# Performance work log

Hardware: AMD Instinct MI355X
Metric: run time of the kernel (lower is better)

## Reference

```python
import jax, jax.numpy as jnp
import numpy as np

L, B, N, C, H = 6, 4, 512, 512, 8
D = C // H          # head_dim = 64
MLP = 4 * C         # mlp_ratio = 4.0
EPS = 1e-6


def setup_inputs() -> dict:
    key = jax.random.key(0)
    ks = jax.random.split(key, 12)
    p = lambda k, sh: jax.random.normal(k, sh, dtype=jnp.float32) * 0.02
    return {
        "x": jax.random.normal(ks[0], (B, N, C), dtype=jnp.float32),
        "time_emb": jax.random.normal(ks[1], (B, C), dtype=jnp.float32),
        "pair_emb": jax.random.normal(ks[2], (B, H, N, N), dtype=jnp.float32) * 0.1,
        "is_padded_mask": jnp.zeros((B, 1, 1, N), dtype=bool),
        # per-block stacked params (leading dim = L blocks)
        "wq": p(ks[3], (L, C, C)),
        "wk": p(ks[4], (L, C, C)),
        "wv": p(ks[5], (L, C, C)),
        "wo": p(ks[6], (L, C, C)),
        "bo": jnp.zeros((L, C), dtype=jnp.float32),
        "w1": p(ks[7], (L, C, MLP)),
        "b1": jnp.zeros((L, MLP), dtype=jnp.float32),
        "w2": p(ks[8], (L, MLP, C)),
        "b2": jnp.zeros((L, C), dtype=jnp.float32),
        "wada": p(ks[9], (L, C, 6 * C)),
        "bada": jnp.zeros((L, 6 * C), dtype=jnp.float32),
    }


def _ln(x):
    # LayerNorm without affine, eps=1e-6 (torch elementwise_affine=False)
    mu = jnp.mean(x, axis=-1, keepdims=True)
    var = jnp.mean(jnp.square(x - mu), axis=-1, keepdims=True)
    return (x - mu) * jax.lax.rsqrt(var + EPS)


def _modulate(x, shift, scale):
    return x * (1.0 + scale[:, None, :]) + shift[:, None, :]


def reference(x, time_emb, pair_emb, is_padded_mask,
              wq, wk, wv, wo, bo, w1, b1, w2, b2, wada, bada):
    scale = D ** -0.5
    t_act = jax.nn.silu(time_emb)  # shared SiLU input to adaLN of each block
    for i in range(L):
        ada = t_act @ wada[i] + bada[i]  # (B, 6C)
        sh_msa, sc_msa, g_msa, sh_mlp, sc_mlp, g_mlp = jnp.split(ada, 6, axis=1)
        # fill_attn_mask: masked_fill padded key positions with -inf
        pair = jnp.where(is_padded_mask, -jnp.inf, pair_emb)  # (B,H,N,N)
        mx = _modulate(_ln(x), sh_msa, sc_msa)  # (B,N,C)
        q = (mx @ wq[i]).reshape(B, N, H, D)
        k = (mx @ wk[i]).reshape(B, N, H, D)
        v = (mx @ wv[i]).reshape(B, N, H, D)
        qk = jnp.einsum('bnhd,bshd->bhns', q, k) * scale  # (B,H,N,N)
        attn = jax.nn.softmax(qk + pair, axis=-1)
        o = jnp.einsum('bhns,bshd->bnhd', attn, v).reshape(B, N, C)
        o = o @ wo[i] + bo[i]
        x = x + g_msa[:, None, :] * o
        pair_emb = pair + qk  # residual on pair embedding
        h = _modulate(_ln(x), sh_mlp, sc_mlp)
        h = jax.nn.gelu(h @ w1[i] + b1[i], approximate=True) @ w2[i] + b2[i]
        x = x + g_mlp[:, None, :] * h
    return x, pair_emb
```

## Files before the change

### kernel.cpp

```cpp
#include <hip/hip_runtime.h>
#include <hip/hip_bf16.h>

#define LNUM 6
#define BB 4
#define NSEQ 512
#define CDIM 512
#define HNUM 8
#define DHEAD 64
#define MLPD 2048
#define MROWS (BB*NSEQ)

typedef __hip_bfloat16 bf16;
typedef __attribute__((ext_vector_type(4))) float f32x4;
typedef __attribute__((ext_vector_type(8))) short bf16x8;

__device__ __forceinline__ void gld_lds16(const bf16* g, bf16* l) {
  __builtin_amdgcn_global_load_lds((const __attribute__((address_space(1))) void*)g,
                                   (__attribute__((address_space(3))) void*)l, 16, 0, 0);
}

__device__ __forceinline__ short f2bs(float f) {
  bf16 h = __float2bfloat16(f);
  short s; __builtin_memcpy(&s, &h, 2); return s;
}

__device__ __forceinline__ float gelu_tanh(float t) {
  float u = 0.7978845608028654f * (t + 0.044715f * t * t * t);
  u = fminf(fmaxf(u, -15.f), 15.f);
  float e = __expf(2.f * u);
  return 0.5f * t * (1.f + (e - 1.f) / (e + 1.f));
}

enum { EP_BF16 = 0, EP_SCORES = 1, EP_RESID = 2, EP_GELU = 3 };

template<int MODE>
__global__ __launch_bounds__(256) void gemm_nt(
    const bf16* __restrict__ A, int lda,
    const bf16* __restrict__ Bt, int ldb,
    int K, int zdiv,
    long sA1, long sA2, long sB1, long sB2, long sO1, long sO2,
    bf16* __restrict__ obf, float* __restrict__ of32, int ldo,
    const float* __restrict__ bias,
    const float* __restrict__ ada, int gate_off,
    float* __restrict__ xres,
    const float* __restrict__ pair_in,
    const unsigned char* __restrict__ mask,
    float scale)
{
  __shared__ bf16 lA[2 * 64 * 64];
  __shared__ bf16 lB[2 * 64 * 64];
  const int tid = threadIdx.x;
  const int wid = tid >> 6, lane = tid & 63;
  const int z = blockIdx.z;
  const long z1 = z / zdiv, z2 = z % zdiv;
  A  += z1 * sA1 + z2 * sA2;
  Bt += z1 * sB1 + z2 * sB2;
  const long obase = z1 * sO1 + z2 * sO2;
  const int m0 = blockIdx.x * 64;
  const int n0 = blockIdx.y * 64;
  const int wm = wid >> 1, wn = wid & 1;
  const int srow = tid >> 3, scl = tid & 7;

  f32x4 zero = {0.f, 0.f, 0.f, 0.f};
  f32x4 acc[2][2];
#pragma unroll
  for (int i = 0; i < 2; i++)
#pragma unroll
    for (int j = 0; j < 2; j++) acc[i][j] = zero;

  auto stage = [&](int buf, int kt) {
#pragma unroll
    for (int r = 0; r < 2; r++) {
      const int rr = (r << 5) + srow;
      const int gk = (scl ^ (rr & 7)) << 3;
      gld_lds16(A + (size_t)(m0 + rr) * lda + (kt << 6) + gk,
                lA + buf * 4096 + (r << 11) + (wid << 9));
    }
#pragma unroll
    for (int r = 0; r < 2; r++) {
      const int rr = (r << 5) + srow;
      const int gk = (scl ^ (rr & 7)) << 3;
      gld_lds16(Bt + (size_t)(n0 + rr) * ldb + (kt << 6) + gk,
                lB + buf * 4096 + (r << 11) + (wid << 9));
    }
  };

  const int rlo = lane & 15, kq = lane >> 4;
  auto compute = [&](int buf) {
    bf16x8 af[2][2], bg[2][2];
#pragma unroll
    for (int kk = 0; kk < 2; kk++) {
#pragma unroll
      for (int i = 0; i < 2; i++) {
        const int ra = (wm << 5) + (i << 4) + rlo;
        af[kk][i] = *(const bf16x8*)(lA + buf * 4096 + (ra << 6) +
                                     ((((kk << 2) + kq) ^ (ra & 7)) << 3));
        const int rb2 = (wn << 5) + (i << 4) + rlo;
        bg[kk][i] = *(const bf16x8*)(lB + buf * 4096 + (rb2 << 6) +
                                     ((((kk << 2) + kq) ^ (rb2 & 7)) << 3));
      }
    }
#pragma unroll
    for (int kk = 0; kk < 2; kk++)
#pragma unroll
      for (int i = 0; i < 2; i++)
#pragma unroll
        for (int j = 0; j < 2; j++)
          acc[i][j] = __builtin_amdgcn_mfma_f32_16x16x32_bf16(af[kk][i], bg[kk][j], acc[i][j], 0, 0, 0);
  };

  const int NT = K >> 6;
  stage(0, 0);
  for (int t = 0; t < NT - 1; t++) {
    stage((t + 1) & 1, t + 1);
    asm volatile("s_waitcnt vmcnt(4)" ::: "memory");
    __builtin_amdgcn_s_barrier();
    asm volatile("" ::: "memory");
    compute(t & 1);
    asm volatile("" ::: "memory");
    __builtin_amdgcn_s_barrier();
  }
  asm volatile("s_waitcnt vmcnt(0)" ::: "memory");
  __builtin_amdgcn_s_barrier();
  asm volatile("" ::: "memory");
  compute((NT - 1) & 1);

  const int cl = lane & 15, rb = (lane >> 4) << 2;
#pragma unroll
  for (int i = 0; i < 2; i++) {
#pragma unroll
    for (int j = 0; j < 2; j++) {
      const int gc = n0 + (wn << 5) + (j << 4) + cl;
#pragma unroll
      for (int r = 0; r < 4; r++) {
        const int gr = m0 + (wm << 5) + (i << 4) + rb + r;
        float v = acc[i][j][r];
        if (MODE == EP_BF16) {
          obf[obase + (size_t)gr * ldo + gc] = __float2bfloat16(v);
        } else if (MODE == EP_SCORES) {
          float pr = pair_in[obase + (size_t)gr * ldo + gc];
          if (mask[z1 * NSEQ + gc]) pr = -INFINITY;
          of32[obase + (size_t)gr * ldo + gc] = pr + v * scale;
        } else if (MODE == EP_RESID) {
          const int b = gr >> 9;
          float t2 = v + bias[gc];
          xres[(size_t)gr * CDIM + gc] += ada[b * (6 * CDIM) + gate_off + gc] * t2;
        } else {
          float t2 = v + bias[gc];
          obf[obase + (size_t)gr * ldo + gc] = __float2bfloat16(gelu_tanh(t2));
        }
      }
    }
  }
}

__global__ __launch_bounds__(256) void ln_mod(const float* __restrict__ x,
                                              const float* __restrict__ ada,
                                              int sh_off, int sc_off,
                                              bf16* __restrict__ out)
{
  const int row = blockIdx.x;
  const int b = row >> 9;
  const float* xr = x + (size_t)row * CDIM;
  const int t = threadIdx.x;
  float2 v = ((const float2*)xr)[t];
  float s = v.x + v.y;
  float ss = v.x * v.x + v.y * v.y;
#pragma unroll
  for (int o = 32; o > 0; o >>= 1) { s += __shfl_down(s, o); ss += __shfl_down(ss, o); }
  __shared__ float red[8];
  __shared__ float mv[2];
  const int w = t >> 6, ln = t & 63;
  if (ln == 0) { red[w] = s; red[4 + w] = ss; }
  __syncthreads();
  if (t == 0) {
    float S = red[0] + red[1] + red[2] + red[3];
    float SS = red[4] + red[5] + red[6] + red[7];
    float mu = S * (1.0f / CDIM);
    float var = SS * (1.0f / CDIM) - mu * mu;
    mv[0] = mu; mv[1] = rsqrtf(var + 1e-6f);
  }
  __syncthreads();
  const float mu = mv[0], rs = mv[1];
  const float* adab = ada + b * (6 * CDIM);
  const int c = t * 2;
  float o0 = (v.x - mu) * rs * (1.0f + adab[sc_off + c])     + adab[sh_off + c];
  float o1 = (v.y - mu) * rs * (1.0f + adab[sc_off + c + 1]) + adab[sh_off + c + 1];
  out[(size_t)row * CDIM + c]     = __float2bfloat16(o0);
  out[(size_t)row * CDIM + c + 1] = __float2bfloat16(o1);
}

__global__ __launch_bounds__(256) void ada_gemm(const float* __restrict__ te,
                                                const float* __restrict__ wada,
                                                const float* __restrict__ bada,
                                                float* __restrict__ out)
{
  __shared__ float ta[CDIM];
  const int layer = blockIdx.y;
  const float* wada_i = wada + (size_t)layer * CDIM * 6 * CDIM;
  const float* bada_i = bada + (size_t)layer * 6 * CDIM;
  float* out_i = out + (size_t)layer * BB * 6 * CDIM;
  const int idx = blockIdx.x * 256 + threadIdx.x;
  const int b = idx / (6 * CDIM);
  const int col = idx % (6 * CDIM);
  for (int i = threadIdx.x; i < CDIM; i += 256) {
    float xx = te[b * CDIM + i];
    ta[i] = xx / (1.f + __expf(-xx));
  }
  __syncthreads();
  float acc = bada_i[col];
#pragma unroll 8
  for (int k = 0; k < CDIM; k++)
    acc = fmaf(ta[k], wada_i[(size_t)k * (6 * CDIM) + col], acc);
  out_i[idx] = acc;
}

__global__ __launch_bounds__(64) void softmax_rows(const float* __restrict__ S,
                                                   bf16* __restrict__ P)
{
  const size_t row = blockIdx.x;
  const float* sr = S + row * NSEQ;
  const int t = threadIdx.x;
  float4 a = ((const float4*)sr)[t];
  float4 b = ((const float4*)sr)[t + 64];
  float m = fmaxf(fmaxf(fmaxf(a.x, a.y), fmaxf(a.z, a.w)),
                  fmaxf(fmaxf(b.x, b.y), fmaxf(b.z, b.w)));
#pragma unroll
  for (int o = 32; o > 0; o >>= 1) m = fmaxf(m, __shfl_xor(m, o));
  float e0 = __expf(a.x - m), e1 = __expf(a.y - m), e2 = __expf(a.z - m), e3 = __expf(a.w - m);
  float e4 = __expf(b.x - m), e5 = __expf(b.y - m), e6 = __expf(b.z - m), e7 = __expf(b.w - m);
  float sum = (e0 + e1 + e2 + e3) + (e4 + e5 + e6 + e7);
#pragma unroll
  for (int o = 32; o > 0; o >>= 1) sum += __shfl_xor(sum, o);
  const float inv = 1.0f / sum;
  short4 w0, w1;
  w0.x = f2bs(e0 * inv); w0.y = f2bs(e1 * inv); w0.z = f2bs(e2 * inv); w0.w = f2bs(e3 * inv);
  w1.x = f2bs(e4 * inv); w1.y = f2bs(e5 * inv); w1.z = f2bs(e6 * inv); w1.w = f2bs(e7 * inv);
  bf16* pr = P + row * NSEQ;
  ((short4*)pr)[t] = w0;
  ((short4*)pr)[t + 64] = w1;
}

__global__ __launch_bounds__(256) void conv_t(const float* __restrict__ src, bf16* __restrict__ dst,
                                              int R, int Ccols, long sS, long sD)
{
  src += (size_t)blockIdx.z * sS;
  dst += (size_t)blockIdx.z * sD;
  __shared__ float tb[32][33];
  const int c0 = blockIdx.x * 32, r0 = blockIdx.y * 32;
  const int tx = threadIdx.x & 31, ty = threadIdx.x >> 5;
#pragma unroll
  for (int i = ty; i < 32; i += 8) tb[i][tx] = src[(size_t)(r0 + i) * Ccols + c0 + tx];
  __syncthreads();
#pragma unroll
  for (int i = ty; i < 32; i += 8) dst[(size_t)(c0 + i) * R + r0 + tx] = __float2bfloat16(tb[tx][i]);
}

__global__ __launch_bounds__(256) void vtrans(const bf16* __restrict__ qkv, bf16* __restrict__ vt)
{
  const int z = blockIdx.z, b = z >> 3, h = z & 7;
  const bf16* src = qkv + (size_t)b * NSEQ * 1536 + 2 * CDIM + h * DHEAD;
  bf16* dst = vt + (size_t)z * DHEAD * NSEQ;
  __shared__ bf16 tb[32][33];
  const int n0 = blockIdx.x * 32, d0 = blockIdx.y * 32;
  const int tx = threadIdx.x & 31, ty = threadIdx.x >> 5;
#pragma unroll
  for (int i = ty; i < 32; i += 8) tb[i][tx] = src[(size_t)(n0 + i) * 1536 + d0 + tx];
  __syncthreads();
#pragma unroll
  for (int i = ty; i < 32; i += 8) dst[(size_t)(d0 + i) * NSEQ + n0 + tx] = tb[tx][i];
}

extern "C" void kernel_launch(void* const* d_in, const int* in_sizes, int n_in,
                              void* d_out, int out_size, void* d_ws, size_t ws_size,
                              hipStream_t stream)
{
  (void)in_sizes; (void)n_in; (void)out_size; (void)ws_size;
  const float* in_x    = (const float*)d_in[0];
  const float* in_te   = (const float*)d_in[1];
  const float* in_pair = (const float*)d_in[2];
  const unsigned char* in_mask = (const unsigned char*)d_in[3];
  const float* wq   = (const float*)d_in[4];
  const float* wk   = (const float*)d_in[5];
  const float* wv   = (const float*)d_in[6];
  const float* wo   = (const float*)d_in[7];
  const float* bo   = (const float*)d_in[8];
  const float* w1   = (const float*)d_in[9];
  const float* b1   = (const float*)d_in[10];
  const float* w2   = (const float*)d_in[11];
  const float* b2   = (const float*)d_in[12];
  const float* wada = (const float*)d_in[13];
  const float* bada = (const float*)d_in[14];

  float* xout = (float*)d_out;
  float* pairout = xout + (size_t)BB * NSEQ * CDIM;

  char* ws = (char*)d_ws;
  size_t off = 0;
  auto alloc = [&](size_t bytes) -> void* {
    void* p = ws + off; off += (bytes + 255) & ~(size_t)255; return p;
  };
  bf16*  wqkvT = (bf16*)alloc((size_t)LNUM * 1536 * 512 * 2);
  bf16*  woT   = (bf16*)alloc((size_t)LNUM * 512 * 512 * 2);
  bf16*  w1T   = (bf16*)alloc((size_t)LNUM * 2048 * 512 * 2);
  bf16*  w2T   = (bf16*)alloc((size_t)LNUM * 512 * 2048 * 2);
  float* adab  = (float*)alloc((size_t)LNUM * BB * 6 * CDIM * 4);
  bf16*  mx    = (bf16*)alloc((size_t)MROWS * CDIM * 2);
  bf16*  qkv   = (bf16*)alloc((size_t)MROWS * 1536 * 2);
  bf16*  vt    = (bf16*)alloc((size_t)BB * HNUM * DHEAD * NSEQ * 2);
  bf16*  Pbuf  = (bf16*)alloc((size_t)BB * HNUM * NSEQ * NSEQ * 2);
  bf16*  obuf  = (bf16*)alloc((size_t)MROWS * CDIM * 2);
  bf16*  hbuf  = (bf16*)alloc((size_t)MROWS * MLPD * 2);

  hipMemcpyAsync(xout, in_x, (size_t)MROWS * CDIM * 4, hipMemcpyDeviceToDevice, stream);

  conv_t<<<dim3(16, 16, LNUM), 256, 0, stream>>>(wq, wqkvT,               512, 512,  (long)512 * 512,  (long)1536 * 512);
  conv_t<<<dim3(16, 16, LNUM), 256, 0, stream>>>(wk, wqkvT + 512 * 512,   512, 512,  (long)512 * 512,  (long)1536 * 512);
  conv_t<<<dim3(16, 16, LNUM), 256, 0, stream>>>(wv, wqkvT + 2 * 512 * 512, 512, 512, (long)512 * 512, (long)1536 * 512);
  conv_t<<<dim3(16, 16, LNUM), 256, 0, stream>>>(wo, woT,                 512, 512,  (long)512 * 512,  (long)512 * 512);
  conv_t<<<dim3(64, 16, LNUM), 256, 0, stream>>>(w1, w1T,                 512, 2048, (long)512 * 2048, (long)2048 * 512);
  conv_t<<<dim3(16, 64, LNUM), 256, 0, stream>>>(w2, w2T,                 2048, 512, (long)2048 * 512, (long)512 * 2048);

  ada_gemm<<<dim3(BB * 6 * CDIM / 256, LNUM), 256, 0, stream>>>(in_te, wada, bada, adab);

  const float scale = 0.125f;
  for (int i = 0; i < LNUM; i++) {
    const float* adal = adab + (size_t)i * BB * 6 * CDIM;
    ln_mod<<<MROWS, 256, 0, stream>>>(xout, adal, 0, CDIM, mx);
    gemm_nt<EP_BF16><<<dim3(32, 24, 1), 256, 0, stream>>>(
        mx, CDIM, wqkvT + (size_t)i * 1536 * 512, CDIM, CDIM, 1,
        0, 0, 0, 0, 0, 0,
        qkv, nullptr, 1536,
        nullptr, nullptr, 0, nullptr, nullptr, nullptr, 0.f);
    vtrans<<<dim3(16, 2, 32), 256, 0, stream>>>(qkv, vt);
    const float* pin = (i == 0) ? in_pair : pairout;
    gemm_nt<EP_SCORES><<<dim3(8, 8, 32), 256, 0, stream>>>(
        qkv, 1536, qkv + CDIM, 1536, DHEAD, HNUM,
        (long)NSEQ * 1536, 64, (long)NSEQ * 1536, 64,
        (long)HNUM * NSEQ * NSEQ, (long)NSEQ * NSEQ,
        nullptr, pairout, NSEQ,
        nullptr, nullptr, 0, nullptr, pin, in_mask, scale);
    softmax_rows<<<dim3(BB * HNUM * NSEQ), 64, 0, stream>>>(pairout, Pbuf);
    gemm_nt<EP_BF16><<<dim3(8, 1, 32), 256, 0, stream>>>(
        Pbuf, NSEQ, vt, NSEQ, NSEQ, HNUM,
        (long)HNUM * NSEQ * NSEQ, (long)NSEQ * NSEQ,
        (long)HNUM * DHEAD * NSEQ, (long)DHEAD * NSEQ,
        (long)NSEQ * CDIM, DHEAD,
        obuf, nullptr, CDIM,
        nullptr, nullptr, 0, nullptr, nullptr, nullptr, 0.f);
    gemm_nt<EP_RESID><<<dim3(32, 8, 1), 256, 0, stream>>>(
        obuf, CDIM, woT + (size_t)i * CDIM * CDIM, CDIM, CDIM, 1,
        0, 0, 0, 0, 0, 0,
        nullptr, nullptr, CDIM,
        bo + (size_t)i * CDIM, adal, 2 * CDIM, xout, nullptr, nullptr, 0.f);
    ln_mod<<<MROWS, 256, 0, stream>>>(xout, adal, 3 * CDIM, 4 * CDIM, mx);
    gemm_nt<EP_GELU><<<dim3(32, 32, 1), 256, 0, stream>>>(
        mx, CDIM, w1T + (size_t)i * MLPD * CDIM, CDIM, CDIM, 1,
        0, 0, 0, 0, 0, 0,
        hbuf, nullptr, MLPD,
        b1 + (size_t)i * MLPD, nullptr, 0, nullptr, nullptr, nullptr, 0.f);
    gemm_nt<EP_RESID><<<dim3(32, 8, 1), 256, 0, stream>>>(
        hbuf, MLPD, w2T + (size_t)i * CDIM * MLPD, MLPD, MLPD, 1,
        0, 0, 0, 0, 0, 0,
        nullptr, nullptr, CDIM,
        b2 + (size_t)i * CDIM, adal, 5 * CDIM, xout, nullptr, nullptr, 0.f);
  }
}
```

Baseline: 615.3 us.

## Fuse attention scores, online softmax and PV into one flash-style kernel

Replaces the separate scores GEMM, row softmax and P·V GEMM with one kernel per (batch, head, 64-row tile). The kernel streams K/V tiles through double-buffered LDS, adds the pair bias, writes the updated pair embedding, and accumulates the output with an online softmax. This removes the bf16 P round-trip through global memory and two launches per layer. The adaLN GEMM is also split over K into partial and reduce kernels to get more parallelism. The fused grid has only 256 blocks, so the GPU may be undersubscribed.

```diff
diff --git a/kernel.cpp b/kernel.cpp
--- a/kernel.cpp
+++ b/kernel.cpp
@@ -31,7 +31,7 @@
   return 0.5f * t * (1.f + (e - 1.f) / (e + 1.f));
 }
 
-enum { EP_BF16 = 0, EP_SCORES = 1, EP_RESID = 2, EP_GELU = 3 };
+enum { EP_BF16 = 0, EP_RESID = 2, EP_GELU = 3 };
 
 template<int MODE>
 __global__ __launch_bounds__(256) void gemm_nt(
@@ -39,13 +39,10 @@
     const bf16* __restrict__ Bt, int ldb,
     int K, int zdiv,
     long sA1, long sA2, long sB1, long sB2, long sO1, long sO2,
-    bf16* __restrict__ obf, float* __restrict__ of32, int ldo,
+    bf16* __restrict__ obf, int ldo,
     const float* __restrict__ bias,
     const float* __restrict__ ada, int gate_off,
-    float* __restrict__ xres,
-    const float* __restrict__ pair_in,
-    const unsigned char* __restrict__ mask,
-    float scale)
+    float* __restrict__ xres)
 {
   __shared__ bf16 lA[2 * 64 * 64];
   __shared__ bf16 lB[2 * 64 * 64];
@@ -137,10 +134,6 @@
         float v = acc[i][j][r];
         if (MODE == EP_BF16) {
           obf[obase + (size_t)gr * ldo + gc] = __float2bfloat16(v);
-        } else if (MODE == EP_SCORES) {
-          float pr = pair_in[obase + (size_t)gr * ldo + gc];
-          if (mask[z1 * NSEQ + gc]) pr = -INFINITY;
-          of32[obase + (size_t)gr * ldo + gc] = pr + v * scale;
         } else if (MODE == EP_RESID) {
           const int b = gr >> 9;
           float t2 = v + bias[gc];
@@ -152,6 +145,160 @@
       }
     }
   }
+}
+
+__global__ __launch_bounds__(256) void attn_fused(
+    const bf16* __restrict__ qkv, const bf16* __restrict__ vt,
+    const float* __restrict__ pair_in, float* __restrict__ pair_out,
+    const unsigned char* __restrict__ mask,
+    bf16* __restrict__ obuf, float scale)
+{
+  __shared__ bf16 lQ[64 * 64];
+  __shared__ bf16 lK[2][64 * 64];
+  __shared__ bf16 lV[2][64 * 64];
+  __shared__ bf16 lP[64 * 64];
+  const int tid = threadIdx.x, wid = tid >> 6, lane = tid & 63;
+  const int z = blockIdx.z, b = z >> 3, h = z & 7;
+  const int m0 = blockIdx.x * 64;
+  const int srow = tid >> 3, scl = tid & 7;
+  const bf16* Aq = qkv + (size_t)b * NSEQ * 1536 + h * 64;
+  const bf16* Bk = Aq + CDIM;
+  const bf16* Bv = vt + (size_t)z * DHEAD * NSEQ;
+  const size_t pz = (size_t)z * NSEQ * NSEQ;
+
+#pragma unroll
+  for (int r = 0; r < 2; r++) {
+    const int rr = (r << 5) + srow;
+    const int gk = (scl ^ (rr & 7)) << 3;
+    gld_lds16(Aq + (size_t)(m0 + rr) * 1536 + gk, lQ + (r << 11) + (wid << 9));
+    gld_lds16(Bk + (size_t)rr * 1536 + gk, lK[0] + (r << 11) + (wid << 9));
+    gld_lds16(Bv + (size_t)rr * NSEQ + gk, lV[0] + (r << 11) + (wid << 9));
+  }
+
+  const int rlo = lane & 15, kq = lane >> 4, cl = rlo;
+  float m_run[4], l_run[4];
+  f32x4 oacc[4];
+  f32x4 zero = {0.f, 0.f, 0.f, 0.f};
+#pragma unroll
+  for (int r = 0; r < 4; r++) { m_run[r] = -INFINITY; l_run[r] = 0.f; }
+#pragma unroll
+  for (int j = 0; j < 4; j++) oacc[j] = zero;
+  bf16x8 afq[2];
+
+  for (int ct = 0; ct < 8; ct++) {
+    const int cur = ct & 1;
+    asm volatile("s_waitcnt vmcnt(0)" ::: "memory");
+    __builtin_amdgcn_s_barrier();
+    asm volatile("" ::: "memory");
+
+    if (ct < 7) {
+#pragma unroll
+      for (int r = 0; r < 2; r++) {
+        const int rr = (r << 5) + srow;
+        const int gk = (scl ^ (rr & 7)) << 3;
+        gld_lds16(Bk + (size_t)((ct + 1) * 64 + rr) * 1536 + gk,
+                  lK[cur ^ 1] + (r << 11) + (wid << 9));
+        gld_lds16(Bv + (size_t)rr * NSEQ + (ct + 1) * 64 + gk,
+                  lV[cur ^ 1] + (r << 11) + (wid << 9));
+      }
+    }
+
+    if (ct == 0) {
+#pragma unroll
+      for (int kk = 0; kk < 2; kk++) {
+        const int ra = (wid << 4) + rlo;
+        afq[kk] = *(const bf16x8*)(lQ + (ra << 6) + ((((kk << 1) << 1) + kq) == 0 ? 0 : 0));
+      }
+#pragma unroll
+      for (int kk = 0; kk < 2; kk++) {
+        const int ra = (wid << 4) + rlo;
+        afq[kk] = *(const bf16x8*)(lQ + (ra << 6) + ((((kk << 2) + kq) ^ (ra & 7)) << 3));
+      }
+    }
+
+    float pr[4][4];
+#pragma unroll
+    for (int j = 0; j < 4; j++)
+#pragma unroll
+      for (int r = 0; r < 4; r++)
+        pr[j][r] = pair_in[pz + (size_t)(m0 + (wid << 4) + (kq << 2) + r) * NSEQ +
+                           (ct * 64 + (j << 4) + cl)];
+    bool mk[4];
+#pragma unroll
+    for (int j = 0; j < 4; j++)
+      mk[j] = mask[b * NSEQ + ct * 64 + (j << 4) + cl] != 0;
+
+    f32x4 s[4];
+#pragma unroll
+    for (int j = 0; j < 4; j++) s[j] = zero;
+#pragma unroll
+    for (int kk = 0; kk < 2; kk++)
+#pragma unroll
+      for (int j = 0; j < 4; j++) {
+        const int rk = (j << 4) + rlo;
+        bf16x8 bk = *(const bf16x8*)(lK[cur] + (rk << 6) + ((((kk << 2) + kq) ^ (rk & 7)) << 3));
+        s[j] = __builtin_amdgcn_mfma_f32_16x16x32_bf16(afq[kk], bk, s[j], 0, 0, 0);
+      }
+
+    float p[4][4];
+#pragma unroll
+    for (int r = 0; r < 4; r++) {
+      const size_t prow = pz + (size_t)(m0 + (wid << 4) + (kq << 2) + r) * NSEQ + ct * 64;
+      float sf[4];
+#pragma unroll
+      for (int j = 0; j < 4; j++) {
+        float pp = mk[j] ? -INFINITY : pr[j][r];
+        sf[j] = s[j][r] * scale + pp;
+        pair_out[prow + (j << 4) + cl] = sf[j];
+      }
+      float tm = fmaxf(fmaxf(sf[0], sf[1]), fmaxf(sf[2], sf[3]));
+#pragma unroll
+      for (int o = 1; o < 16; o <<= 1) tm = fmaxf(tm, __shfl_xor(tm, o));
+      const float mnew = fmaxf(m_run[r], tm);
+      const float fr = __expf(m_run[r] - mnew);
+      float rs = 0.f;
+#pragma unroll
+      for (int j = 0; j < 4; j++) { p[j][r] = __expf(sf[j] - mnew); rs += p[j][r]; }
+#pragma unroll
+      for (int o = 1; o < 16; o <<= 1) rs += __shfl_xor(rs, o);
+      l_run[r] = l_run[r] * fr + rs;
+      m_run[r] = mnew;
+#pragma unroll
+      for (int j = 0; j < 4; j++) oacc[j][r] *= fr;
+    }
+
+#pragma unroll
+    for (int j = 0; j < 4; j++)
+#pragma unroll
+      for (int r = 0; r < 4; r++) {
+        const int row = (wid << 4) + (kq << 2) + r;
+        const int col = (j << 4) + cl;
+        lP[(row << 6) + (((col >> 3) ^ (row & 7)) << 3) + (col & 7)] = __float2bfloat16(p[j][r]);
+      }
+    asm volatile("s_waitcnt lgkmcnt(0)" ::: "memory");
+    __builtin_amdgcn_sched_barrier(0);
+
+#pragma unroll
+    for (int kk = 0; kk < 2; kk++) {
+      const int ra = (wid << 4) + rlo;
+      bf16x8 ap = *(const bf16x8*)(lP + (ra << 6) + ((((kk << 2) + kq) ^ (ra & 7)) << 3));
+#pragma unroll
+      for (int j = 0; j < 4; j++) {
+        const int rd = (j << 4) + rlo;
+        bf16x8 bv = *(const bf16x8*)(lV[cur] + (rd << 6) + ((((kk << 2) + kq) ^ (rd & 7)) << 3));
+        oacc[j] = __builtin_amdgcn_mfma_f32_16x16x32_bf16(ap, bv, oacc[j], 0, 0, 0);
+      }
+    }
+  }
+
+#pragma unroll
+  for (int j = 0; j < 4; j++)
+#pragma unroll
+    for (int r = 0; r < 4; r++) {
+      const int gr = m0 + (wid << 4) + (kq << 2) + r;
+      const int gc = h * 64 + (j << 4) + cl;
+      obuf[((size_t)b * NSEQ + gr) * CDIM + gc] = __float2bfloat16(oacc[j][r] / l_run[r]);
+    }
 }
 
 __global__ __launch_bounds__(256) void ln_mod(const float* __restrict__ x,
@@ -190,55 +337,49 @@
   out[(size_t)row * CDIM + c + 1] = __float2bfloat16(o1);
 }
 
-__global__ __launch_bounds__(256) void ada_gemm(const float* __restrict__ te,
+__global__ __launch_bounds__(256) void ada_part(const float* __restrict__ te,
                                                 const float* __restrict__ wada,
-                                                const float* __restrict__ bada,
-                                                float* __restrict__ out)
-{
-  __shared__ float ta[CDIM];
-  const int layer = blockIdx.y;
-  const float* wada_i = wada + (size_t)layer * CDIM * 6 * CDIM;
-  const float* bada_i = bada + (size_t)layer * 6 * CDIM;
-  float* out_i = out + (size_t)layer * BB * 6 * CDIM;
+                                                float* __restrict__ partial)
+{
+  __shared__ float ta[4][64];
+  const int layer = blockIdx.z, kc = blockIdx.y;
+  const int t = threadIdx.x;
+  {
+    const int b = t >> 6, kk = t & 63;
+    float xx = te[b * CDIM + kc * 64 + kk];
+    ta[b][kk] = xx / (1.f + __expf(-xx));
+  }
+  __syncthreads();
+  const int col = blockIdx.x * 512 + t * 2;
+  const float* W = wada + ((size_t)layer * CDIM + kc * 64) * 3072 + col;
+  float2 acc0 = {0, 0}, acc1 = {0, 0}, acc2 = {0, 0}, acc3 = {0, 0};
+#pragma unroll 8
+  for (int kk = 0; kk < 64; kk++) {
+    float2 w = *(const float2*)(W + (size_t)kk * 3072);
+    acc0.x = fmaf(ta[0][kk], w.x, acc0.x); acc0.y = fmaf(ta[0][kk], w.y, acc0.y);
+    acc1.x = fmaf(ta[1][kk], w.x, acc1.x); acc1.y = fmaf(ta[1][kk], w.y, acc1.y);
+    acc2.x = fmaf(ta[2][kk], w.x, acc2.x); acc2.y = fmaf(ta[2][kk], w.y, acc2.y);
+    acc3.x = fmaf(ta[3][kk], w.x, acc3.x); acc3.y = fmaf(ta[3][kk], w.y, acc3.y);
+  }
+  float* pp = partial + (((size_t)(layer * 8 + kc) * 4) * 3072);
+  *(float2*)(pp + 0 * 3072 + col) = acc0;
+  *(float2*)(pp + 1 * 3072 + col) = acc1;
+  *(float2*)(pp + 2 * 3072 + col) = acc2;
+  *(float2*)(pp + 3 * 3072 + col) = acc3;
+}
+
+__global__ __launch_bounds__(256) void ada_reduce(const float* __restrict__ partial,
+                                                  const float* __restrict__ bada,
+                                                  float* __restrict__ adab)
+{
   const int idx = blockIdx.x * 256 + threadIdx.x;
-  const int b = idx / (6 * CDIM);
-  const int col = idx % (6 * CDIM);
-  for (int i = threadIdx.x; i < CDIM; i += 256) {
-    float xx = te[b * CDIM + i];
-    ta[i] = xx / (1.f + __expf(-xx));
-  }
-  __syncthreads();
-  float acc = bada_i[col];
-#pragma unroll 8
-  for (int k = 0; k < CDIM; k++)
-    acc = fmaf(ta[k], wada_i[(size_t)k * (6 * CDIM) + col], acc);
-  out_i[idx] = acc;
-}
-
-__global__ __launch_bounds__(64) void softmax_rows(const float* __restrict__ S,
-                                                   bf16* __restrict__ P)
-{
-  const size_t row = blockIdx.x;
-  const float* sr = S + row * NSEQ;
-  const int t = threadIdx.x;
-  float4 a = ((const float4*)sr)[t];
-  float4 b = ((const float4*)sr)[t + 64];
-  float m = fmaxf(fmaxf(fmaxf(a.x, a.y), fmaxf(a.z, a.w)),
-                  fmaxf(fmaxf(b.x, b.y), fmaxf(b.z, b.w)));
-#pragma unroll
-  for (int o = 32; o > 0; o >>= 1) m = fmaxf(m, __shfl_xor(m, o));
-  float e0 = __expf(a.x - m), e1 = __expf(a.y - m), e2 = __expf(a.z - m), e3 = __expf(a.w - m);
-  float e4 = __expf(b.x - m), e5 = __expf(b.y - m), e6 = __expf(b.z - m), e7 = __expf(b.w - m);
-  float sum = (e0 + e1 + e2 + e3) + (e4 + e5 + e6 + e7);
-#pragma unroll
-  for (int o = 32; o > 0; o >>= 1) sum += __shfl_xor(sum, o);
-  const float inv = 1.0f / sum;
-  short4 w0, w1;
-  w0.x = f2bs(e0 * inv); w0.y = f2bs(e1 * inv); w0.z = f2bs(e2 * inv); w0.w = f2bs(e3 * inv);
-  w1.x = f2bs(e4 * inv); w1.y = f2bs(e5 * inv); w1.z = f2bs(e6 * inv); w1.w = f2bs(e7 * inv);
-  bf16* pr = P + row * NSEQ;
-  ((short4*)pr)[t] = w0;
-  ((short4*)pr)[t + 64] = w1;
+  const int layer = idx / 12288, rem = idx % 12288;
+  const int b = rem / 3072, col = rem % 3072;
+  float acc = bada[layer * 3072 + col];
+#pragma unroll
+  for (int kc = 0; kc < 8; kc++)
+    acc += partial[((size_t)(layer * 8 + kc) * 4 + b) * 3072 + col];
+  adab[((size_t)layer * 4 + b) * 3072 + col] = acc;
 }
 
 __global__ __launch_bounds__(256) void conv_t(const float* __restrict__ src, bf16* __restrict__ dst,
@@ -305,10 +446,10 @@
   bf16*  w1T   = (bf16*)alloc((size_t)LNUM * 2048 * 512 * 2);
   bf16*  w2T   = (bf16*)alloc((size_t)LNUM * 512 * 2048 * 2);
   float* adab  = (float*)alloc((size_t)LNUM * BB * 6 * CDIM * 4);
+  float* apart = (float*)alloc((size_t)LNUM * 8 * BB * 3072 * 4);
   bf16*  mx    = (bf16*)alloc((size_t)MROWS * CDIM * 2);
   bf16*  qkv   = (bf16*)alloc((size_t)MROWS * 1536 * 2);
   bf16*  vt    = (bf16*)alloc((size_t)BB * HNUM * DHEAD * NSEQ * 2);
-  bf16*  Pbuf  = (bf16*)alloc((size_t)BB * HNUM * NSEQ * NSEQ * 2);
   bf16*  obuf  = (bf16*)alloc((size_t)MROWS * CDIM * 2);
   bf16*  hbuf  = (bf16*)alloc((size_t)MROWS * MLPD * 2);
 
@@ -321,7 +462,8 @@
   conv_t<<<dim3(64, 16, LNUM), 256, 0, stream>>>(w1, w1T,                 512, 2048, (long)512 * 2048, (long)2048 * 512);
   conv_t<<<dim3(16, 64, LNUM), 256, 0, stream>>>(w2, w2T,                 2048, 512, (long)2048 * 512, (long)512 * 2048);
 
-  ada_gemm<<<dim3(BB * 6 * CDIM / 256, LNUM), 256, 0, stream>>>(in_te, wada, bada, adab);
+  ada_part<<<dim3(6, 8, LNUM), 256, 0, stream>>>(in_te, wada, apart);
+  ada_reduce<<<dim3(LNUM * BB * 3072 / 256), 256, 0, stream>>>(apart, bada, adab);
 
   const float scale = 0.125f;
   for (int i = 0; i < LNUM; i++) {
@@ -330,39 +472,22 @@
     gemm_nt<EP_BF16><<<dim3(32, 24, 1), 256, 0, stream>>>(
         mx, CDIM, wqkvT + (size_t)i * 1536 * 512, CDIM, CDIM, 1,
         0, 0, 0, 0, 0, 0,
-        qkv, nullptr, 1536,
-        nullptr, nullptr, 0, nullptr, nullptr, nullptr, 0.f);
+        qkv, 1536, nullptr, nullptr, 0, nullptr);
     vtrans<<<dim3(16, 2, 32), 256, 0, stream>>>(qkv, vt);
     const float* pin = (i == 0) ? in_pair : pairout;
-    gemm_nt<EP_SCORES><<<dim3(8, 8, 32), 256, 0, stream>>>(
-        qkv, 1536, qkv + CDIM, 1536, DHEAD, HNUM,
-        (long)NSEQ * 1536, 64, (long)NSEQ * 1536, 64,
-        (long)HNUM * NSEQ * NSEQ, (long)NSEQ * NSEQ,
-        nullptr, pairout, NSEQ,
-        nullptr, nullptr, 0, nullptr, pin, in_mask, scale);
-    softmax_rows<<<dim3(BB * HNUM * NSEQ), 64, 0, stream>>>(pairout, Pbuf);
-    gemm_nt<EP_BF16><<<dim3(8, 1, 32), 256, 0, stream>>>(
-        Pbuf, NSEQ, vt, NSEQ, NSEQ, HNUM,
-        (long)HNUM * NSEQ * NSEQ, (long)NSEQ * NSEQ,
-        (long)HNUM * DHEAD * NSEQ, (long)DHEAD * NSEQ,
-        (long)NSEQ * CDIM, DHEAD,
-        obuf, nullptr, CDIM,
-        nullptr, nullptr, 0, nullptr, nullptr, nullptr, 0.f);
+    attn_fused<<<dim3(8, 1, 32), 256, 0, stream>>>(qkv, vt, pin, pairout, in_mask, obuf, scale);
     gemm_nt<EP_RESID><<<dim3(32, 8, 1), 256, 0, stream>>>(
         obuf, CDIM, woT + (size_t)i * CDIM * CDIM, CDIM, CDIM, 1,
         0, 0, 0, 0, 0, 0,
-        nullptr, nullptr, CDIM,
-        bo + (size_t)i * CDIM, adal, 2 * CDIM, xout, nullptr, nullptr, 0.f);
+        nullptr, CDIM, bo + (size_t)i * CDIM, adal, 2 * CDIM, xout);
     ln_mod<<<MROWS, 256, 0, stream>>>(xout, adal, 3 * CDIM, 4 * CDIM, mx);
     gemm_nt<EP_GELU><<<dim3(32, 32, 1), 256, 0, stream>>>(
         mx, CDIM, w1T + (size_t)i * MLPD * CDIM, CDIM, CDIM, 1,
         0, 0, 0, 0, 0, 0,
-        hbuf, nullptr, MLPD,
-        b1 + (size_t)i * MLPD, nullptr, 0, nullptr, nullptr, nullptr, 0.f);
+        hbuf, MLPD, b1 + (size_t)i * MLPD, nullptr, 0, nullptr);
     gemm_nt<EP_RESID><<<dim3(32, 8, 1), 256, 0, stream>>>(
         hbuf, MLPD, w2T + (size_t)i * CDIM * MLPD, MLPD, MLPD, 1,
         0, 0, 0, 0, 0, 0,
-        nullptr, nullptr, CDIM,
-        b2 + (size_t)i * CDIM, adal, 5 * CDIM, xout, nullptr, nullptr, 0.f);
-  }
-}
+        nullptr, CDIM, b2 + (size_t)i * CDIM, adal, 5 * CDIM, xout);
+  }
+}
```

Result: faster. 542.5 us (-11.8%).
